# Kernel tuning notes

Hardware: AMD Instinct MI355X
Metric: run time of the kernel (lower is better)

The kernel has to match this reference:

```python
import jax, jax.numpy as jnp
import numpy as np

B, S, D, H = 2, 2048, 1024, 16
DK = D // H

def setup_inputs() -> dict:
    key = jax.random.key(0)
    ks = jax.random.split(key, 11)
    scale = 1.0 / np.sqrt(D)
    inp = {
        'q': jax.random.normal(ks[0], (B, S, D), jnp.float32),
        'k': jax.random.normal(ks[1], (B, S, D), jnp.float32),
        'v': jax.random.normal(ks[2], (B, S, D), jnp.float32),
        'mask': jnp.ones((1, 1, S, S), jnp.int32),
        'Wq': jax.random.normal(ks[3], (D, D), jnp.float32) * scale,
        'bq': jnp.zeros((D,), jnp.float32),
        'Wk': jax.random.normal(ks[4], (D, D), jnp.float32) * scale,
        'bk': jnp.zeros((D,), jnp.float32),
        'Wv': jax.random.normal(ks[5], (D, D), jnp.float32) * scale,
        'bv': jnp.zeros((D,), jnp.float32),
        'Wo': jax.random.normal(ks[6], (D, D), jnp.float32) * scale,
        'bo': jnp.zeros((D,), jnp.float32),
    }
    return inp

def reference(q, k, v, mask, Wq, bq, Wk, bk, Wv, bv, Wo, bo):
    # Linear projections, split into heads: [B,S,D] -> [B,H,S,DK]
    def proj(x, W, b):
        return (x @ W + b).reshape(B, -1, H, DK).transpose(0, 2, 1, 3)
    Q = proj(q, Wq, bq)
    K = proj(k, Wk, bk)
    V = proj(v, Wv, bv)
    scores = jnp.einsum('bhqd,bhkd->bhqk', Q, K) / jnp.sqrt(jnp.float32(DK))
    scores = jnp.where(mask == 0, jnp.float32(-1e9), scores)
    attn = jax.nn.softmax(scores, axis=-1)  # dropout is identity in eval mode
    out = jnp.einsum('bhqk,bhkd->bhqd', attn, V)
    out = out.transpose(0, 2, 1, 3).reshape(B, -1, D)
    return out @ Wo + bo
```

## Files before the change

### kernel.cpp

```cpp
#include <hip/hip_runtime.h>
#include <stdint.h>

#define B_  2
#define S_  2048
#define D_  1024
#define H_  16
#define M_  (B_*S_)

typedef __attribute__((ext_vector_type(8)))  short  short8;
typedef __attribute__((ext_vector_type(4)))  float  floatx4;
typedef __attribute__((ext_vector_type(16))) float  floatx16;
typedef __attribute__((ext_vector_type(4)))  float  f32x4;
typedef __attribute__((ext_vector_type(8)))  unsigned short u16x8;
typedef __attribute__((ext_vector_type(4)))  unsigned short u16x4;
typedef __attribute__((ext_vector_type(2)))  unsigned int   uint2v;

#define LOG2E_  1.44269504088896f
#define QSCALE_ (0.125f * LOG2E_)

__device__ __forceinline__ unsigned short f2bf(float x){
  union { float f; uint32_t u; } v; v.f = x;
  uint32_t r = v.u + 0x7FFFu + ((v.u >> 16) & 1u);
  return (unsigned short)(r >> 16);
}

__device__ __forceinline__ uint32_t cvt_pk_bf16(float lo, float hi){
  uint32_t r;
  asm("v_cvt_pk_bf16_f32 %0, %1, %2" : "=v"(r) : "v"(lo), "v"(hi));
  return r;
}

__device__ __forceinline__ void pl32swap(uint32_t &a, uint32_t &b){
#if __has_builtin(__builtin_amdgcn_permlane32_swap)
  uint2v r = __builtin_amdgcn_permlane32_swap(a, b, false, false);
  a = r[0]; b = r[1];
#else
  const int hi = (threadIdx.x & 63) >> 5;
  uint32_t sa = (uint32_t)__shfl_xor((int)a, 32);
  uint32_t sb = (uint32_t)__shfl_xor((int)b, 32);
  uint32_t na = hi ? sb : a;
  uint32_t nb = hi ? b  : sa;
  a = na; b = nb;
#endif
}

#define GLL16(G, L) __builtin_amdgcn_global_load_lds( \
    (const __attribute__((address_space(1))) void*)(G), \
    (__attribute__((address_space(3))) void*)(L), 16, 0, 0)

__global__ __launch_bounds__(256) void k_wt4(const float* __restrict__ Wq,
        const float* __restrict__ Wk, const float* __restrict__ Wv, const float* __restrict__ Wo,
        unsigned short* __restrict__ wqt, unsigned short* __restrict__ wkt,
        unsigned short* __restrict__ wvt, unsigned short* __restrict__ wot){
  const int z = blockIdx.z;
  const float* W = z==0 ? Wq : z==1 ? Wk : z==2 ? Wv : Wo;
  unsigned short* Wt = z==0 ? wqt : z==1 ? wkt : z==2 ? wvt : wot;
  __shared__ float tile[32][33];
  int n0 = blockIdx.x*32, k0 = blockIdx.y*32;
  int tx = threadIdx.x, ty = threadIdx.y;
  #pragma unroll
  for (int i=0;i<32;i+=8) tile[ty+i][tx] = W[(size_t)(k0+ty+i)*D_ + n0+tx];
  __syncthreads();
  #pragma unroll
  for (int i=0;i<32;i+=8) Wt[(size_t)(n0+ty+i)*D_ + k0+tx] = f2bf(tile[tx][ty+i]);
}

__global__ __launch_bounds__(256,3) void k_gemm_qkv(
        const float* __restrict__ q, const float* __restrict__ k, const float* __restrict__ v,
        const unsigned short* __restrict__ wqt, const unsigned short* __restrict__ wkt,
        const unsigned short* __restrict__ wvt,
        const float* __restrict__ bq, const float* __restrict__ bk, const float* __restrict__ bv,
        unsigned short* __restrict__ Qp, unsigned short* __restrict__ Kp,
        unsigned short* __restrict__ Vt)
{
  __shared__ __align__(16) unsigned short As[128*32];
  __shared__ __align__(16) unsigned short Bs[128*32];
  const int z = blockIdx.z;
  const float* A = z==0 ? q : z==1 ? k : v;
  const unsigned short* Bt = z==0 ? wqt : z==1 ? wkt : wvt;
  const float* bias = z==0 ? bq : z==1 ? bk : bv;
  const float scale = z==0 ? QSCALE_ : 1.0f;

  const int tid = threadIdx.x;
  const int lane = tid & 63, wid = tid >> 6;
  const int wr = wid >> 1, wc = wid & 1;
  const int row0 = blockIdx.y*128, col0 = blockIdx.x*128;
  const int l15 = lane & 15, l4 = lane >> 4;

  const int arow = tid >> 1, ak = (tid & 1)*16;
  const float* aptr = A + (size_t)(row0 + arow)*D_ + ak;

  f32x4 ar0 = *(const f32x4*)(aptr+0), ar1 = *(const f32x4*)(aptr+4),
        ar2 = *(const f32x4*)(aptr+8), ar3 = *(const f32x4*)(aptr+12);

  floatx4 acc[4][4];
  #pragma unroll
  for (int i=0;i<4;i++)
    #pragma unroll
    for (int j=0;j<4;j++)
      #pragma unroll
      for (int r=0;r<4;r++) acc[i][j][r] = 0.f;

  for (int k0=0; k0<D_; k0+=32){
    __syncthreads();
    #pragma unroll
    for (int it=0; it<2; it++){
      int idx = it*256 + tid;
      int r = idx >> 2, c = idx & 3;
      GLL16(Bt + (size_t)(col0 + r)*D_ + k0 + c*8, Bs + (size_t)(it*4 + wid)*512);
    }
    union { uint32_t w[8]; short8 s[2]; } aw;
    aw.w[0]=cvt_pk_bf16(ar0[0],ar0[1]); aw.w[1]=cvt_pk_bf16(ar0[2],ar0[3]);
    aw.w[2]=cvt_pk_bf16(ar1[0],ar1[1]); aw.w[3]=cvt_pk_bf16(ar1[2],ar1[3]);
    aw.w[4]=cvt_pk_bf16(ar2[0],ar2[1]); aw.w[5]=cvt_pk_bf16(ar2[2],ar2[3]);
    aw.w[6]=cvt_pk_bf16(ar3[0],ar3[1]); aw.w[7]=cvt_pk_bf16(ar3[2],ar3[3]);
    *(short8*)(As + arow*32 + ak)     = aw.s[0];
    *(short8*)(As + arow*32 + ak + 8) = aw.s[1];
    if (k0 + 32 < D_){
      const float* ap = aptr + k0 + 32;
      ar0 = *(const f32x4*)(ap+0); ar1 = *(const f32x4*)(ap+4);
      ar2 = *(const f32x4*)(ap+8); ar3 = *(const f32x4*)(ap+12);
    }
    __syncthreads();
    short8 af[4], bfr[4];
    #pragma unroll
    for (int i=0;i<4;i++)
      af[i] = *(const short8*)(As + (wr*64 + i*16 + l15)*32 + l4*8);
    #pragma unroll
    for (int j=0;j<4;j++)
      bfr[j] = *(const short8*)(Bs + (wc*64 + j*16 + l15)*32 + l4*8);
    #pragma unroll
    for (int i=0;i<4;i++)
      #pragma unroll
      for (int j=0;j<4;j++)
        acc[i][j] = __builtin_amdgcn_mfma_f32_16x16x32_bf16(af[i], bfr[j], acc[i][j], 0,0,0);
  }

  if (z != 2){
    unsigned short* C = z==0 ? Qp : Kp;
    #pragma unroll
    for (int i=0;i<4;i++){
      #pragma unroll
      for (int j=0;j<4;j++){
        int col = col0 + wc*64 + j*16 + l15;
        float bv_ = bias[col];
        int rowb = row0 + wr*64 + i*16 + l4*4;
        #pragma unroll
        for (int r=0;r<4;r++)
          C[(size_t)(rowb + r)*D_ + col] = f2bf((acc[i][j][r] + bv_) * scale);
      }
    }
  } else {
    #pragma unroll
    for (int i=0;i<4;i++){
      #pragma unroll
      for (int j=0;j<4;j++){
        int col = col0 + wc*64 + j*16 + l15;
        float bv_ = bias[col];
        int rowb = row0 + wr*64 + i*16 + l4*4;
        int bb = rowb >> 11, ss = rowb & 2047;
        u16x4 o;
        #pragma unroll
        for (int r=0;r<4;r++) o[r] = f2bf(acc[i][j][r] + bv_);
        *(u16x4*)(Vt + ((size_t)(bb*1024 + col))*S_ + ss) = o;
      }
    }
  }
}

__global__ __launch_bounds__(256) void k_gemm_out(const unsigned short* __restrict__ A,
        const unsigned short* __restrict__ Bt, const float* __restrict__ bias,
        float* __restrict__ C)
{
  __shared__ __align__(16) unsigned short As[128*32];
  __shared__ __align__(16) unsigned short Bs[128*32];
  const int tid = threadIdx.x;
  const int lane = tid & 63, wid = tid >> 6;
  const int wr = wid >> 1, wc = wid & 1;
  const int row0 = blockIdx.y*128, col0 = blockIdx.x*128;
  const int l15 = lane & 15, l4 = lane >> 4;

  floatx4 acc[4][4];
  #pragma unroll
  for (int i=0;i<4;i++)
    #pragma unroll
    for (int j=0;j<4;j++)
      #pragma unroll
      for (int r=0;r<4;r++) acc[i][j][r] = 0.f;

  for (int k0=0; k0<D_; k0+=32){
    __syncthreads();
    #pragma unroll
    for (int it=0; it<2; it++){
      int idx = it*256 + tid;
      int r = idx >> 2, c = idx & 3;
      GLL16(A  + (size_t)(row0 + r)*D_ + k0 + c*8, As + (size_t)(it*4 + wid)*512);
      GLL16(Bt + (size_t)(col0 + r)*D_ + k0 + c*8, Bs + (size_t)(it*4 + wid)*512);
    }
    __syncthreads();
    short8 af[4], bfr[4];
    #pragma unroll
    for (int i=0;i<4;i++)
      af[i] = *(const short8*)(As + (wr*64 + i*16 + l15)*32 + l4*8);
    #pragma unroll
    for (int j=0;j<4;j++)
      bfr[j] = *(const short8*)(Bs + (wc*64 + j*16 + l15)*32 + l4*8);
    #pragma unroll
    for (int i=0;i<4;i++)
      #pragma unroll
      for (int j=0;j<4;j++)
        acc[i][j] = __builtin_amdgcn_mfma_f32_16x16x32_bf16(af[i], bfr[j], acc[i][j], 0,0,0);
  }

  #pragma unroll
  for (int i=0;i<4;i++){
    #pragma unroll
    for (int j=0;j<4;j++){
      int col = col0 + wc*64 + j*16 + l15;
      float bv_ = bias[col];
      int rowb = row0 + wr*64 + i*16 + l4*4;
      #pragma unroll
      for (int r=0;r<4;r++)
        C[(size_t)(rowb + r)*D_ + col] = acc[i][j][r] + bv_;
    }
  }
}

__global__ __launch_bounds__(256,4) void k_attn(const unsigned short* __restrict__ Qp,
        const unsigned short* __restrict__ Kp, const unsigned short* __restrict__ Vt,
        float* __restrict__ Op, float* __restrict__ Lp)
{
  __shared__ __align__(16) unsigned short smem[16384];
  unsigned short* const kb0 = smem;
  unsigned short* const vb0 = smem + 4096;
  unsigned short* const kb1 = smem + 8192;
  unsigned short* const vb1 = smem + 12288;

  const int sblk = blockIdx.x;
  const int xcd = sblk & 7, jj = sblk >> 3;
  const int bh = xcd + 8*(jj >> 5);
  const int rem = jj & 31, qt = rem >> 1, part = rem & 1;
  const int b = bh >> 4, h = bh & 15;
  const int q0 = qt*128;

  const int tid  = threadIdx.x;
  const int lane = tid & 63, wid = tid >> 6;
  const int lo5  = lane & 31, hi = lane >> 5;
  const int qm = b*S_ + q0 + wid*32 + lo5;

  short8 qf[4];
  #pragma unroll
  for (int f=0; f<4; f++)
    qf[f] = *(const short8*)(Qp + (size_t)qm*D_ + h*64 + f*16 + hi*8);

  floatx16 zv;
  #pragma unroll
  for (int r=0;r<16;r++) zv[r] = 0.f;
  floatx16 ot0 = zv, ot1 = zv;
  float lsum = 0.f;

  const int srow = tid >> 3;
  const int sc   = (tid & 7) ^ (srow & 7);
  const unsigned short* kp0 = Kp + ((size_t)b*S_)*D_ + h*64
                              + (size_t)(part*1024 + srow)*D_ + sc*8;
  const unsigned short* kp1 = kp0 + (size_t)32*D_;
  const unsigned short* vp0 = Vt + ((size_t)(b*1024 + h*64 + srow))*S_ + part*1024 + sc*8;
  const unsigned short* vp1 = vp0 + (size_t)32*S_;

  auto STAGE = [&](unsigned short* kdst, unsigned short* vdst, int tt){
    const size_t ko = (size_t)tt*64*D_;
    const int    vo = tt*64;
    GLL16(kp0 + ko, kdst + wid*512);
    GLL16(kp1 + ko, kdst + (4+wid)*512);
    GLL16(vp0 + vo, vdst + wid*512);
    GLL16(vp1 + vo, vdst + (4+wid)*512);
  };

  const int ksw = lo5 & 7;

  auto COMPUTE = [&](const unsigned short* kbuf, const unsigned short* vbuf){
    floatx16 st0, st1;
    __builtin_amdgcn_s_setprio(1);
    {
      const int cc = hi ^ ksw;
      short8 ka0 = *(const short8*)(kbuf + lo5*64      + cc*8);
      short8 ka1 = *(const short8*)(kbuf + (32+lo5)*64 + cc*8);
      st0 = __builtin_amdgcn_mfma_f32_32x32x16_bf16(ka0, qf[0], zv, 0,0,0);
      st1 = __builtin_amdgcn_mfma_f32_32x32x16_bf16(ka1, qf[0], zv, 0,0,0);
    }
    #pragma unroll
    for (int f=1; f<4; f++){
      const int cc = (2*f + hi) ^ ksw;
      short8 ka0 = *(const short8*)(kbuf + lo5*64      + cc*8);
      short8 ka1 = *(const short8*)(kbuf + (32+lo5)*64 + cc*8);
      st0 = __builtin_amdgcn_mfma_f32_32x32x16_bf16(ka0, qf[f], st0, 0,0,0);
      st1 = __builtin_amdgcn_mfma_f32_32x32x16_bf16(ka1, qf[f], st1, 0,0,0);
    }
    __builtin_amdgcn_s_setprio(0);

    #pragma unroll
    for (int kh=0; kh<2; kh++){
      const floatx16& st = kh ? st1 : st0;
      #pragma unroll
      for (int blk=0; blk<2; blk++){
        const int bs = blk*8;
        float e0 = exp2f(st[bs+0]), e1 = exp2f(st[bs+1]);
        float e2 = exp2f(st[bs+2]), e3 = exp2f(st[bs+3]);
        float e4 = exp2f(st[bs+4]), e5 = exp2f(st[bs+5]);
        float e6 = exp2f(st[bs+6]), e7 = exp2f(st[bs+7]);
        lsum += ((e0+e1)+(e2+e3)) + ((e4+e5)+(e6+e7));
        uint32_t a01 = cvt_pk_bf16(e0,e1);
        uint32_t a23 = cvt_pk_bf16(e2,e3);
        uint32_t a45 = cvt_pk_bf16(e4,e5);
        uint32_t a67 = cvt_pk_bf16(e6,e7);
        pl32swap(a01, a45);
        pl32swap(a23, a67);
        union { uint32_t w[4]; short8 v; } pu;
        pu.w[0] = a01; pu.w[1] = a23; pu.w[2] = a45; pu.w[3] = a67;
        const int kvc = kh*4 + blk*2 + hi;
        {
          const int d = lo5;
          short8 va = *(const short8*)(vbuf + d*64 + ((kvc ^ (d&7))*8));
          ot0 = __builtin_amdgcn_mfma_f32_32x32x16_bf16(va, pu.v, ot0, 0,0,0);
        }
        {
          const int d = 32 + lo5;
          short8 va = *(const short8*)(vbuf + d*64 + ((kvc ^ (d&7))*8));
          ot1 = __builtin_amdgcn_mfma_f32_32x32x16_bf16(va, pu.v, ot1, 0,0,0);
        }
      }
    }
  };

  STAGE(kb0, vb0, 0);
  __syncthreads();
  #pragma unroll 1
  for (int t2=0; t2<8; ++t2){
    const int tt = t2*2;
    STAGE(kb1, vb1, tt+1);
    COMPUTE(kb0, vb0);
    __syncthreads();
    if (t2 < 7) STAGE(kb0, vb0, tt+2);
    COMPUTE(kb1, vb1);
    __syncthreads();
  }

  lsum += __shfl_xor(lsum, 32);
  if (hi == 0)
    Lp[(size_t)part*65536 + (size_t)h*4096 + qm] = lsum;

  float* ob = Op + ((size_t)part << 22);
  #pragma unroll
  for (int r=0;r<16;r++){
    const int d = (r&3) + 8*(r>>2) + 4*hi;
    ob[(size_t)(h*64 + d)*4096      + qm] = ot0[r];
    ob[(size_t)(h*64 + d + 32)*4096 + qm] = ot1[r];
  }
}

__global__ __launch_bounds__(256) void k_combine(const float* __restrict__ Op,
        const float* __restrict__ Lp, unsigned short* __restrict__ Of)
{
  __shared__ float tile[64*68];
  __shared__ float linv[64];
  const int bx = blockIdx.x;
  const int mt = bx & 63, h = bx >> 6;
  const int m0 = mt*64, d0 = h*64;
  const int t = threadIdx.x;

  if (t < 64){
    float l0 = Lp[(size_t)h*4096 + m0 + t];
    float l1 = Lp[65536 + (size_t)h*4096 + m0 + t];
    linv[t] = 1.0f / (l0 + l1);
  }
  __syncthreads();

  const int dd = t >> 2, mc = t & 3;
  const float* p0 = Op + (size_t)(d0 + dd)*4096 + m0 + mc*16;
  const float* p1 = p0 + 4194304;
  #pragma unroll
  for (int i=0;i<4;i++){
    f32x4 a = *(const f32x4*)(p0 + i*4);
    f32x4 bb = *(const f32x4*)(p1 + i*4);
    f32x4 iv = *(const f32x4*)(linv + mc*16 + i*4);
    f32x4 vv = (a + bb) * iv;
    *(f32x4*)(tile + dd*68 + mc*16 + i*4) = vv;
  }
  __syncthreads();

  const int mm = t >> 2, dc = t & 3;
  u16x8 o0, o1;
  #pragma unroll
  for (int j=0;j<8;j++) o0[j] = f2bf(tile[(dc*16 + j)*68 + mm]);
  #pragma unroll
  for (int j=0;j<8;j++) o1[j] = f2bf(tile[(dc*16 + 8 + j)*68 + mm]);
  *(u16x8*)(Of + (size_t)(m0 + mm)*1024 + d0 + dc*16)     = o0;
  *(u16x8*)(Of + (size_t)(m0 + mm)*1024 + d0 + dc*16 + 8) = o1;
}

extern "C" void kernel_launch(void* const* d_in, const int* in_sizes, int n_in,
                              void* d_out, int out_size, void* d_ws, size_t ws_size,
                              hipStream_t stream)
{
  (void)in_sizes; (void)n_in; (void)out_size; (void)ws_size;
  const float* q  = (const float*)d_in[0];
  const float* k  = (const float*)d_in[1];
  const float* v  = (const float*)d_in[2];
  const float* Wq = (const float*)d_in[4];
  const float* bq = (const float*)d_in[5];
  const float* Wk = (const float*)d_in[6];
  const float* bk = (const float*)d_in[7];
  const float* Wv = (const float*)d_in[8];
  const float* bv = (const float*)d_in[9];
  const float* Wo = (const float*)d_in[10];
  const float* bo = (const float*)d_in[11];

  char* ws = (char*)d_ws;
  unsigned short* Qp  = (unsigned short*)(ws + 0);
  unsigned short* Kp  = (unsigned short*)(ws + 8388608);
  unsigned short* Vt  = (unsigned short*)(ws + 16777216);
  float*          Op  = (float*)        (ws + 25165824);
  unsigned short* wqt = (unsigned short*)(ws + 58720256);
  unsigned short* wkt = (unsigned short*)(ws + 60817408);
  unsigned short* wvt = (unsigned short*)(ws + 62914560);
  unsigned short* wot = (unsigned short*)(ws + 65011712);
  float*          Lp  = (float*)        (ws + 67108864);
  unsigned short* Of  = Qp;

  k_wt4<<<dim3(D_/32, D_/32, 4), dim3(32,8), 0, stream>>>(Wq, Wk, Wv, Wo,
                                                          wqt, wkt, wvt, wot);

  k_gemm_qkv<<<dim3(D_/128, M_/128, 3), 256, 0, stream>>>(q, k, v, wqt, wkt, wvt,
                                                          bq, bk, bv, Qp, Kp, Vt);

  k_attn<<<dim3(1024), 256, 0, stream>>>(Qp, Kp, Vt, Op, Lp);

  k_combine<<<dim3(1024), 256, 0, stream>>>(Op, Lp, Of);

  k_gemm_out<<<dim3(D_/128, M_/128), 256, 0, stream>>>(Of, wot, bo, (float*)d_out);
}
```

Measured before the change: 152.8 us.

## Pre-convert QKV inputs to bf16 and remap GEMM blocks per XCD

Adds a separate kernel that converts q, k, v from fp32 to bf16, so the QKV GEMM can load A tiles with direct global-to-LDS loads instead of register-staged fp32 loads and in-loop conversion. Both GEMMs now use a flattened 1D grid whose block index is remapped so that consecutive blocks on the same XCD share row panels, aiming for better L2 reuse. The cost is an extra launch plus a full fp32 read and bf16 write of the activations, and the workspace layout is reshuffled with aliased buffers.

```diff
diff --git a/kernel.cpp b/kernel.cpp
--- a/kernel.cpp
+++ b/kernel.cpp
@@ -48,6 +48,22 @@
     (const __attribute__((address_space(1))) void*)(G), \
     (__attribute__((address_space(3))) void*)(L), 16, 0, 0)
 
+__global__ __launch_bounds__(256) void k_cvt3(const float* __restrict__ q,
+        const float* __restrict__ k, const float* __restrict__ v,
+        unsigned short* __restrict__ qb, unsigned short* __restrict__ kb,
+        unsigned short* __restrict__ vb){
+  const int z = blockIdx.y;
+  const float* src = z==0 ? q : z==1 ? k : v;
+  unsigned short* dst = z==0 ? qb : z==1 ? kb : vb;
+  int i = blockIdx.x*256 + threadIdx.x;
+  f32x4 a = ((const f32x4*)src)[i*2];
+  f32x4 b = ((const f32x4*)src)[i*2+1];
+  u16x8 o;
+  o[0]=f2bf(a[0]); o[1]=f2bf(a[1]); o[2]=f2bf(a[2]); o[3]=f2bf(a[3]);
+  o[4]=f2bf(b[0]); o[5]=f2bf(b[1]); o[6]=f2bf(b[2]); o[7]=f2bf(b[3]);
+  ((u16x8*)dst)[i] = o;
+}
+
 __global__ __launch_bounds__(256) void k_wt4(const float* __restrict__ Wq,
         const float* __restrict__ Wk, const float* __restrict__ Wv, const float* __restrict__ Wo,
         unsigned short* __restrict__ wqt, unsigned short* __restrict__ wkt,
@@ -65,8 +81,9 @@
   for (int i=0;i<32;i+=8) Wt[(size_t)(n0+ty+i)*D_ + k0+tx] = f2bf(tile[tx][ty+i]);
 }
 
-__global__ __launch_bounds__(256,3) void k_gemm_qkv(
-        const float* __restrict__ q, const float* __restrict__ k, const float* __restrict__ v,
+__global__ __launch_bounds__(256) void k_gemm_qkv(
+        const unsigned short* __restrict__ qb, const unsigned short* __restrict__ kb,
+        const unsigned short* __restrict__ vb,
         const unsigned short* __restrict__ wqt, const unsigned short* __restrict__ wkt,
         const unsigned short* __restrict__ wvt,
         const float* __restrict__ bq, const float* __restrict__ bk, const float* __restrict__ bv,
@@ -75,23 +92,22 @@
 {
   __shared__ __align__(16) unsigned short As[128*32];
   __shared__ __align__(16) unsigned short Bs[128*32];
-  const int z = blockIdx.z;
-  const float* A = z==0 ? q : z==1 ? k : v;
+
+  const int bid = blockIdx.x;
+  const int xcd = bid & 7, i2 = bid >> 3;
+  const int cb  = i2 & 7;
+  const int p   = i2 >> 3;
+  const int z   = p >> 2;
+  const int row0 = (xcd + (p & 3)*8) * 128, col0 = cb * 128;
+
+  const unsigned short* A  = z==0 ? qb  : z==1 ? kb  : vb;
   const unsigned short* Bt = z==0 ? wqt : z==1 ? wkt : wvt;
-  const float* bias = z==0 ? bq : z==1 ? bk : bv;
-  const float scale = z==0 ? QSCALE_ : 1.0f;
+  const float* bias        = z==0 ? bq  : z==1 ? bk  : bv;
 
   const int tid = threadIdx.x;
   const int lane = tid & 63, wid = tid >> 6;
   const int wr = wid >> 1, wc = wid & 1;
-  const int row0 = blockIdx.y*128, col0 = blockIdx.x*128;
   const int l15 = lane & 15, l4 = lane >> 4;
-
-  const int arow = tid >> 1, ak = (tid & 1)*16;
-  const float* aptr = A + (size_t)(row0 + arow)*D_ + ak;
-
-  f32x4 ar0 = *(const f32x4*)(aptr+0), ar1 = *(const f32x4*)(aptr+4),
-        ar2 = *(const f32x4*)(aptr+8), ar3 = *(const f32x4*)(aptr+12);
 
   floatx4 acc[4][4];
   #pragma unroll
@@ -107,19 +123,8 @@
     for (int it=0; it<2; it++){
       int idx = it*256 + tid;
       int r = idx >> 2, c = idx & 3;
+      GLL16(A  + (size_t)(row0 + r)*D_ + k0 + c*8, As + (size_t)(it*4 + wid)*512);
       GLL16(Bt + (size_t)(col0 + r)*D_ + k0 + c*8, Bs + (size_t)(it*4 + wid)*512);
-    }
-    union { uint32_t w[8]; short8 s[2]; } aw;
-    aw.w[0]=cvt_pk_bf16(ar0[0],ar0[1]); aw.w[1]=cvt_pk_bf16(ar0[2],ar0[3]);
-    aw.w[2]=cvt_pk_bf16(ar1[0],ar1[1]); aw.w[3]=cvt_pk_bf16(ar1[2],ar1[3]);
-    aw.w[4]=cvt_pk_bf16(ar2[0],ar2[1]); aw.w[5]=cvt_pk_bf16(ar2[2],ar2[3]);
-    aw.w[6]=cvt_pk_bf16(ar3[0],ar3[1]); aw.w[7]=cvt_pk_bf16(ar3[2],ar3[3]);
-    *(short8*)(As + arow*32 + ak)     = aw.s[0];
-    *(short8*)(As + arow*32 + ak + 8) = aw.s[1];
-    if (k0 + 32 < D_){
-      const float* ap = aptr + k0 + 32;
-      ar0 = *(const f32x4*)(ap+0); ar1 = *(const f32x4*)(ap+4);
-      ar2 = *(const f32x4*)(ap+8); ar3 = *(const f32x4*)(ap+12);
     }
     __syncthreads();
     short8 af[4], bfr[4];
@@ -138,6 +143,7 @@
 
   if (z != 2){
     unsigned short* C = z==0 ? Qp : Kp;
+    const float scale = z==0 ? QSCALE_ : 1.0f;
     #pragma unroll
     for (int i=0;i<4;i++){
       #pragma unroll
@@ -174,10 +180,14 @@
 {
   __shared__ __align__(16) unsigned short As[128*32];
   __shared__ __align__(16) unsigned short Bs[128*32];
+
+  const int bid = blockIdx.x;
+  const int xcd = bid & 7, i2 = bid >> 3;
+  const int row0 = (xcd + (i2 >> 3)*8) * 128, col0 = (i2 & 7) * 128;
+
   const int tid = threadIdx.x;
   const int lane = tid & 63, wid = tid >> 6;
   const int wr = wid >> 1, wc = wid & 1;
-  const int row0 = blockIdx.y*128, col0 = blockIdx.x*128;
   const int l15 = lane & 15, l4 = lane >> 4;
 
   floatx4 acc[4][4];
@@ -419,23 +429,28 @@
   unsigned short* Qp  = (unsigned short*)(ws + 0);
   unsigned short* Kp  = (unsigned short*)(ws + 8388608);
   unsigned short* Vt  = (unsigned short*)(ws + 16777216);
-  float*          Op  = (float*)        (ws + 25165824);
-  unsigned short* wqt = (unsigned short*)(ws + 58720256);
-  unsigned short* wkt = (unsigned short*)(ws + 60817408);
-  unsigned short* wvt = (unsigned short*)(ws + 62914560);
-  unsigned short* wot = (unsigned short*)(ws + 65011712);
-  float*          Lp  = (float*)        (ws + 67108864);
-  unsigned short* Of  = Qp;
-
+  unsigned short* qb  = (unsigned short*)(ws + 25165824);
+  unsigned short* kb  = (unsigned short*)(ws + 33554432);
+  unsigned short* vb  = (unsigned short*)(ws + 41943040);
+  unsigned short* wqt = (unsigned short*)(ws + 50331648);
+  unsigned short* wkt = (unsigned short*)(ws + 52428800);
+  unsigned short* wvt = (unsigned short*)(ws + 54525952);
+  unsigned short* wot = (unsigned short*)(ws + 67108864);
+  float*          Lp  = (float*)         (ws + 69206016);
+  float*          Op  = (float*)         (ws + 33554432);
+  unsigned short* Of  = qb;
+
+  const int n8 = M_*D_/8;
+  k_cvt3<<<dim3(n8/256, 3), 256, 0, stream>>>(q, k, v, qb, kb, vb);
   k_wt4<<<dim3(D_/32, D_/32, 4), dim3(32,8), 0, stream>>>(Wq, Wk, Wv, Wo,
                                                           wqt, wkt, wvt, wot);
 
-  k_gemm_qkv<<<dim3(D_/128, M_/128, 3), 256, 0, stream>>>(q, k, v, wqt, wkt, wvt,
-                                                          bq, bk, bv, Qp, Kp, Vt);
+  k_gemm_qkv<<<dim3(768), 256, 0, stream>>>(qb, kb, vb, wqt, wkt, wvt,
+                                            bq, bk, bv, Qp, Kp, Vt);
 
   k_attn<<<dim3(1024), 256, 0, stream>>>(Qp, Kp, Vt, Op, Lp);
 
   k_combine<<<dim3(1024), 256, 0, stream>>>(Op, Lp, Of);
 
-  k_gemm_out<<<dim3(D_/128, M_/128), 256, 0, stream>>>(Of, wot, bo, (float*)d_out);
-}
+  k_gemm_out<<<dim3(256), 256, 0, stream>>>(Of, wot, bo, (float*)d_out);
+}
```

Result: no change. 151.4 us (-1.0%).
